# Optimization experiments

Measured on AMD Instinct MI355X. Metric: run time of the kernel, lower is better.

The kernel has to match this reference:

```python
import jax, jax.numpy as jnp
import numpy as np

D_MODEL = 1024
N_HEADS = 16
D_K = D_MODEL // N_HEADS


def setup_inputs() -> dict:
    key = jax.random.key(0)
    ks = jax.random.split(key, 7)
    B, S, D = 2, 2048, D_MODEL
    scale = 1.0 / np.sqrt(D)
    return {
        "query": jax.random.normal(ks[0], (B, S, D), dtype=jnp.float32),
        "key": jax.random.normal(ks[1], (B, S, D), dtype=jnp.float32),
        "value": jax.random.normal(ks[2], (B, S, D), dtype=jnp.float32),
        "w_q": jax.random.normal(ks[3], (D, D), dtype=jnp.float32) * scale,
        "w_k": jax.random.normal(ks[4], (D, D), dtype=jnp.float32) * scale,
        "w_v": jax.random.normal(ks[5], (D, D), dtype=jnp.float32) * scale,
        "w_o": jax.random.normal(ks[6], (D, D), dtype=jnp.float32) * scale,
    }


def reference(query, key, value, w_q, w_k, w_v, w_o):
    B, S, D = query.shape
    H, Dk = N_HEADS, D_K
    # nn.Linear (no bias): x @ W.T ; then split heads -> [B, H, S, Dk]
    def split_heads(x, W):
        return (x @ W.T).reshape(B, S, H, Dk).transpose(0, 2, 1, 3)
    Q = split_heads(query, w_q)
    K = split_heads(key, w_k)
    V = split_heads(value, w_v)
    scores = jnp.einsum("bhqd,bhkd->bhqk", Q, K) / np.sqrt(Dk).astype(jnp.float32)
    attn = jax.nn.softmax(scores, axis=-1)  # dropout is identity in eval
    attended = jnp.einsum("bhqk,bhkd->bhqd", attn, V)
    attended = attended.transpose(0, 2, 1, 3).reshape(B, S, D)
    output = attended @ w_o.T
    avg_attention = attn.mean(axis=1)  # mean over heads -> [B, S, S]
    return (output, avg_attention)
```

## Files before the change

### kernel.cpp

```cpp
#include <hip/hip_runtime.h>
#include <math.h>

#define SEQ 2048
#define DMODEL 1024
#define NH 16
#define DK 64
#define BATCH 2

using bf16x8 = __attribute__((ext_vector_type(8))) __bf16;
using bf16x4 = __attribute__((ext_vector_type(4))) __bf16;
using f32x4  = __attribute__((ext_vector_type(4))) float;

__device__ inline f32x4 mfma16(bf16x8 a, bf16x8 b, f32x4 c) {
    return __builtin_amdgcn_mfma_f32_16x16x32_bf16(a, b, c, 0, 0, 0);
}

__device__ inline void load_lds16(const void* g, void* l) {
    __builtin_amdgcn_global_load_lds(
        (const __attribute__((address_space(1))) void*)g,
        (__attribute__((address_space(3))) void*)l, 16, 0, 0);
}

#define VMCNT(n) asm volatile("s_waitcnt vmcnt(" #n ")" ::: "memory")
#define BARRIER() __builtin_amdgcn_s_barrier()
#define CFENCE() asm volatile("" ::: "memory")
#define EXP_SCALE 0.18033688011112042f
#define EXP2(x) __builtin_amdgcn_exp2f(x)

__global__ __launch_bounds__(256) void conv_bf16(
        const float* __restrict__ q, const float* __restrict__ k,
        const float* __restrict__ v, const float* __restrict__ wq,
        const float* __restrict__ wk, const float* __restrict__ wv,
        const float* __restrict__ wo,
        __bf16* __restrict__ oq, __bf16* __restrict__ ok, __bf16* __restrict__ ov,
        __bf16* __restrict__ owq, __bf16* __restrict__ owk,
        __bf16* __restrict__ owv, __bf16* __restrict__ owo) {
    int bid = blockIdx.x;
    const float* src;
    __bf16* dst;
    size_t off;
    if (bid < 3072) {
        int ti = bid >> 10;
        src = ti == 0 ? q : (ti == 1 ? k : v);
        dst = ti == 0 ? oq : (ti == 1 ? ok : ov);
        off = (size_t)(bid & 1023) * 4096;
    } else {
        int ti = (bid - 3072) >> 8;
        src = ti == 0 ? wq : (ti == 1 ? wk : (ti == 2 ? wv : wo));
        dst = ti == 0 ? owq : (ti == 1 ? owk : (ti == 2 ? owv : owo));
        off = (size_t)((bid - 3072) & 255) * 4096;
    }
    src += off; dst += off;
    const int t = threadIdx.x;
#pragma unroll
    for (int i = 0; i < 4; ++i) {
        float4 x = *(const float4*)(src + t * 4 + i * 1024);
        bf16x4 y;
        y[0] = (__bf16)x.x; y[1] = (__bf16)x.y;
        y[2] = (__bf16)x.z; y[3] = (__bf16)x.w;
        *(bf16x4*)(dst + t * 4 + i * 1024) = y;
    }
}

__device__ __forceinline__ void gemm_core(const __bf16* __restrict__ A,
                                          const __bf16* __restrict__ B,
                                          void* __restrict__ out, int mode,
                                          int m0, int n0, int N,
                                          __bf16* As, __bf16* Bs) {
    const int t    = threadIdx.x;
    const int w    = t >> 6;
    const int lane = t & 63;
    const int m    = lane & 15;
    const int kg   = lane >> 4;
    const int wr   = w >> 1, wc = w & 1;

    auto stage = [&](int buf, int k0) {
        const __bf16* ga0 = A + (size_t)(m0 + w * 16 + m) * 1024 + k0 + kg * 8;
        load_lds16(ga0, &As[buf * 4096 + w * 512]);
        const __bf16* ga1 = A + (size_t)(m0 + (w + 4) * 16 + m) * 1024 + k0 + kg * 8;
        load_lds16(ga1, &As[buf * 4096 + (w + 4) * 512]);
        const __bf16* gb0 = B + (size_t)(n0 + w * 16 + m) * 1024 + k0 + kg * 8;
        load_lds16(gb0, &Bs[buf * 4096 + w * 512]);
        const __bf16* gb1 = B + (size_t)(n0 + (w + 4) * 16 + m) * 1024 + k0 + kg * 8;
        load_lds16(gb1, &Bs[buf * 4096 + (w + 4) * 512]);
    };

    f32x4 acc[4][4] = {};

    stage(0, 0);
    CFENCE();
    stage(1, 32);

    int cb = 0, sb = 2;
    for (int ts = 0; ts < 32; ++ts) {
        if (ts < 30) {
            stage(sb, (ts + 2) * 32);
            VMCNT(8);
        } else if (ts == 30) {
            VMCNT(4);
        } else {
            VMCNT(0);
        }
        BARRIER();
        CFENCE();
        const __bf16* Ac = &As[cb * 4096];
        const __bf16* Bc = &Bs[cb * 4096];
        bf16x8 af[4], bg[4];
#pragma unroll
        for (int i = 0; i < 4; ++i)
            af[i] = *(const bf16x8*)&Ac[(wr * 4 + i) * 512 + lane * 8];
#pragma unroll
        for (int j = 0; j < 4; ++j)
            bg[j] = *(const bf16x8*)&Bc[(wc * 4 + j) * 512 + lane * 8];
        __builtin_amdgcn_s_setprio(1);
#pragma unroll
        for (int i = 0; i < 4; ++i)
#pragma unroll
            for (int j = 0; j < 4; ++j)
                acc[i][j] = mfma16(af[i], bg[j], acc[i][j]);
        __builtin_amdgcn_s_setprio(0);
        BARRIER();
        cb = cb == 2 ? 0 : cb + 1;
        sb = sb == 2 ? 0 : sb + 1;
    }

#pragma unroll
    for (int i = 0; i < 4; ++i) {
        const int rb = m0 + wr * 64 + i * 16 + kg * 4;
#pragma unroll
        for (int j = 0; j < 4; ++j) {
            const int gc = n0 + wc * 64 + j * 16 + m;
#pragma unroll
            for (int r = 0; r < 4; ++r) {
                const int gr = rb + r;
                const float vv = acc[i][j][r];
                if (mode == 0) {
                    ((float*)out)[(size_t)gr * N + gc] = vv;
                } else if (mode == 1) {
                    ((__bf16*)out)[(size_t)gr * N + gc] = (__bf16)vv;
                } else {
                    const int hh = gr >> 6, dd = gr & 63;
                    const int bb = gc >> 11, ss = gc & 2047;
                    ((__bf16*)out)[(((size_t)bb * NH + hh) * DK + dd) * SEQ + ss] = (__bf16)vv;
                }
            }
        }
    }
}

__device__ __forceinline__ int xcd_swz(int s, int cpx) {
    return (s & 7) * cpx + (s >> 3);
}

__global__ __launch_bounds__(256, 3) void gemm_qkv(
        const __bf16* __restrict__ Xq, const __bf16* __restrict__ Wq, __bf16* Qr,
        const __bf16* __restrict__ Xk, const __bf16* __restrict__ Wk, __bf16* Kr,
        const __bf16* __restrict__ Xv, const __bf16* __restrict__ Wv, __bf16* Vt) {
    __shared__ __align__(16) __bf16 As[12288];
    __shared__ __align__(16) __bf16 Bs[12288];
    const int bid = blockIdx.x;
    if (bid < 256) {
        const int s = xcd_swz(bid, 32);
        gemm_core(Xq, Wq, Qr, 1, (s >> 3) * 128, (s & 7) * 128, 1024, As, Bs);
    } else if (bid < 512) {
        const int s = xcd_swz(bid - 256, 32);
        gemm_core(Xk, Wk, Kr, 1, (s >> 3) * 128, (s & 7) * 128, 1024, As, Bs);
    } else {
        const int s = xcd_swz(bid - 512, 32);
        gemm_core(Wv, Xv, Vt, 2, (s >> 5) * 128, (s & 31) * 128, 4096, As, Bs);
    }
}

__global__ __launch_bounds__(256, 4) void attn_flash(const __bf16* __restrict__ Qr,
                                                     const __bf16* __restrict__ Kr,
                                                     const __bf16* __restrict__ Vt,
                                                     __bf16* __restrict__ att,
                                                     float* __restrict__ invs) {
    __shared__ __align__(16) unsigned char smem[32768];
    __bf16* Kb = (__bf16*)smem;
    __bf16* Vb = Kb + 8192;

    const int t    = threadIdx.x;
    const int w    = t >> 6;
    const int lane = t & 63;
    const int m    = lane & 15;
    const int kg   = lane >> 4;

    const int L  = xcd_swz(blockIdx.x, 128);
    const int b  = L >> 9;
    const int h  = (L >> 5) & 15;
    const int qw = (L & 31) * 64 + w * 16;

    const __bf16* Kh = Kr + (size_t)b * SEQ * 1024 + h * 64;
    const __bf16* Vh = Vt + ((size_t)b * NH + h) * DK * SEQ;

    const size_t rowQ = (size_t)(b * SEQ + qw + m) * 1024 + h * 64 + kg * 8;
    const bf16x8 qa = *(const bf16x8*)(Qr + rowQ);
    const bf16x8 qb = *(const bf16x8*)(Qr + rowQ + 32);
    CFENCE();

    auto kaddr = [&](int bk, int kt) {
        const int p = bk >> 1, dh = bk & 1, i = lane & 15;
        const int key = (p >> 1) * 32 + ((i >> 2) * 8) + (p & 1) * 4 + (i & 3);
        return (const void*)(Kh + (size_t)(kt + key) * 1024 + dh * 32 + (lane >> 4) * 8);
    };
    auto vaddr = [&](int bk, int kt) {
        const int nt = bk >> 1, kv = bk & 1, i = lane & 15;
        return (const void*)(Vh + (size_t)(nt * 16 + i) * SEQ + kt + kv * 32 + (lane >> 4) * 8);
    };
    auto stage = [&](int buf, int kt) {
        load_lds16(kaddr(w, kt),     Kb + buf * 4096 + w * 512);
        load_lds16(kaddr(w + 4, kt), Kb + buf * 4096 + (w + 4) * 512);
        load_lds16(vaddr(w, kt),     Vb + buf * 4096 + w * 512);
        load_lds16(vaddr(w + 4, kt), Vb + buf * 4096 + (w + 4) * 512);
    };

    f32x4 pv[4] = {};
    float rsum = 0.f;

    stage(0, 0);
    CFENCE();
    stage(1, 64);

    int cur = 0;
    for (int ts = 0; ts < 32; ++ts) {
        if (ts < 31) { VMCNT(4); } else { VMCNT(0); }
        BARRIER();
        CFENCE();
        const __bf16* Kc = Kb + cur * 4096;
        const __bf16* Vc = Vb + cur * 4096;
        bf16x4 pk[4];
#pragma unroll
        for (int p = 0; p < 4; ++p) {
            bf16x8 k0 = *(const bf16x8*)&Kc[(p * 2 + 0) * 512 + lane * 8];
            bf16x8 k1 = *(const bf16x8*)&Kc[(p * 2 + 1) * 512 + lane * 8];
            f32x4 c = {};
            c = mfma16(k0, qa, c);
            c = mfma16(k1, qb, c);
            bf16x4 t4;
#pragma unroll
            for (int r = 0; r < 4; ++r) {
                float pe = EXP2(c[r] * EXP_SCALE);
                rsum += pe;
                t4[r] = (__bf16)pe;
            }
            pk[p] = t4;
        }
#pragma unroll
        for (int ks = 0; ks < 2; ++ks) {
            bf16x8 pa;
#pragma unroll
            for (int e = 0; e < 4; ++e) {
                pa[e]     = pk[2 * ks][e];
                pa[4 + e] = pk[2 * ks + 1][e];
            }
#pragma unroll
            for (int nt = 0; nt < 4; ++nt) {
                bf16x8 vb = *(const bf16x8*)&Vc[(nt * 2 + ks) * 512 + lane * 8];
                pv[nt] = mfma16(pa, vb, pv[nt]);
            }
        }
        BARRIER();
        if (ts + 2 < 32) stage(cur, (ts + 2) * 64);
        cur ^= 1;
    }

    rsum += __shfl_xor(rsum, 16);
    rsum += __shfl_xor(rsum, 32);
    const float inv = 1.0f / rsum;
    float* sinv = (float*)(smem + 17408);
    if (lane < 16) {
        sinv[w * 16 + m] = inv;
        invs[((size_t)b * NH + h) * SEQ + qw + m] = inv;
    }
    __syncthreads();
    float iv[4];
#pragma unroll
    for (int r = 0; r < 4; ++r) iv[r] = sinv[w * 16 + kg * 4 + r];

    float* scf = (float*)smem + w * 1088;
#pragma unroll
    for (int nt = 0; nt < 4; ++nt)
#pragma unroll
        for (int r = 0; r < 4; ++r)
            scf[(kg * 4 + r) * 68 + nt * 16 + m] = pv[nt][r] * iv[r];
    __syncthreads();
    {
        const int q = lane >> 2, c0 = (lane & 3) * 16;
        const float* srcf = &scf[q * 68 + c0];
        bf16x8 o0, o1;
#pragma unroll
        for (int j = 0; j < 8; ++j) {
            o0[j] = (__bf16)srcf[j];
            o1[j] = (__bf16)srcf[j + 8];
        }
        __bf16* dst = att + (size_t)(b * SEQ + qw + q) * DMODEL + h * DK + c0;
        *(bf16x8*)(dst)     = o0;
        *(bf16x8*)(dst + 8) = o1;
    }
}

__device__ __forceinline__ void avg_core(const __bf16* __restrict__ Qr,
                                         const __bf16* __restrict__ Kr,
                                         const float* __restrict__ invs,
                                         float* __restrict__ avg,
                                         int L, __bf16* Kb) {
    const int t    = threadIdx.x;
    const int w    = t >> 6;
    const int lane = t & 63;
    const int m    = lane & 15;
    const int kg   = lane >> 4;
    const int b    = L >> 9;
    const int s0   = ((L >> 5) & 15) * 128;
    const int qw   = (L & 31) * 64 + w * 16;

    const __bf16* Kbase = Kr + (size_t)(b * SEQ + s0) * 1024;

    auto stageK = [&](int buf, int h) {
#pragma unroll
        for (int s = 0; s < 4; ++s) {
            const int bk = w * 4 + s;
            const int nt = bk >> 1, dh = bk & 1;
            load_lds16(Kbase + (size_t)(nt * 16 + (lane & 15)) * 1024 + h * 64 +
                           dh * 32 + (lane >> 4) * 8,
                       Kb + buf * 8192 + bk * 512);
        }
    };

    f32x4 acc[8] = {};

    stageK(0, 0);
    const size_t qoff = (size_t)(b * SEQ + qw + m) * 1024 + kg * 8;
    bf16x8 a0 = *(const bf16x8*)(Qr + qoff);
    bf16x8 a1 = *(const bf16x8*)(Qr + qoff + 32);
    f32x4 ivr = *(const f32x4*)&invs[(size_t)b * NH * SEQ + qw + kg * 4];
    __syncthreads();

    int cur = 0;
    for (int h = 0; h < NH; ++h) {
        if (h + 1 < NH) stageK(cur ^ 1, h + 1);
        bf16x8 na0, na1;
        f32x4 nivr;
        if (h + 1 < NH) {
            na0  = *(const bf16x8*)(Qr + qoff + (h + 1) * 64);
            na1  = *(const bf16x8*)(Qr + qoff + (h + 1) * 64 + 32);
            nivr = *(const f32x4*)&invs[((size_t)b * NH + h + 1) * SEQ + qw + kg * 4];
        }
        const __bf16* Kc = Kb + cur * 8192;
#pragma unroll
        for (int nt = 0; nt < 8; ++nt) {
            bf16x8 k0 = *(const bf16x8*)&Kc[(nt * 2 + 0) * 512 + lane * 8];
            bf16x8 k1 = *(const bf16x8*)&Kc[(nt * 2 + 1) * 512 + lane * 8];
            f32x4 c = {};
            c = mfma16(a0, k0, c);
            c = mfma16(a1, k1, c);
#pragma unroll
            for (int r = 0; r < 4; ++r)
                acc[nt][r] += ivr[r] * EXP2(c[r] * EXP_SCALE);
        }
        __syncthreads();
        cur ^= 1;
        a0 = na0; a1 = na1; ivr = nivr;
    }

    const float sc = 1.0f / NH;
#pragma unroll
    for (int nt = 0; nt < 8; ++nt)
#pragma unroll
        for (int r = 0; r < 4; ++r)
            avg[(size_t)(b * SEQ + qw + kg * 4 + r) * SEQ + s0 + nt * 16 + m] =
                acc[nt][r] * sc;
}

__global__ __launch_bounds__(256, 3) void gemm_wo_avg(
        const __bf16* __restrict__ At, const __bf16* __restrict__ Wo,
        float* __restrict__ out,
        const __bf16* __restrict__ Qr, const __bf16* __restrict__ Kr,
        const float* __restrict__ invs, float* __restrict__ avg) {
    __shared__ __align__(16) __bf16 sm[24576];
    const int bid = blockIdx.x;
    if (bid < 256) {
        const int s = xcd_swz(bid, 32);
        gemm_core(At, Wo, out, 0, (s >> 3) * 128, (s & 7) * 128, 1024,
                  sm, sm + 12288);
    } else {
        avg_core(Qr, Kr, invs, avg, xcd_swz(bid - 256, 128), sm);
    }
}

extern "C" void kernel_launch(void* const* d_in, const int* in_sizes, int n_in,
                              void* d_out, int out_size, void* d_ws, size_t ws_size,
                              hipStream_t stream) {
    const float* query = (const float*)d_in[0];
    const float* key   = (const float*)d_in[1];
    const float* value = (const float*)d_in[2];
    const float* w_q   = (const float*)d_in[3];
    const float* w_k   = (const float*)d_in[4];
    const float* w_v   = (const float*)d_in[5];
    const float* w_o   = (const float*)d_in[6];

    float* out = (float*)d_out;
    float* avg = out + (size_t)BATCH * SEQ * DMODEL;

    __bf16* Xq = (__bf16*)d_ws;
    __bf16* Xk = Xq + 4194304;
    __bf16* Xv = Xk + 4194304;
    __bf16* Wq = Xv + 4194304;
    __bf16* Wk = Wq + 1048576;
    __bf16* Wv = Wk + 1048576;
    __bf16* Wo = Wv + 1048576;
    __bf16* Qr = Wo + 1048576;
    __bf16* Kr = Qr + 4194304;
    __bf16* Vt = Kr + 4194304;
    float*  Invs = (float*)(Vt + 4194304);
    __bf16* At = Xq;

    conv_bf16<<<4096, 256, 0, stream>>>(query, key, value, w_q, w_k, w_v, w_o,
                                        Xq, Xk, Xv, Wq, Wk, Wv, Wo);

    gemm_qkv<<<768, 256, 0, stream>>>(Xq, Wq, Qr, Xk, Wk, Kr, Xv, Wv, Vt);

    attn_flash<<<1024, 256, 0, stream>>>(Qr, Kr, Vt, At, Invs);

    gemm_wo_avg<<<1280, 256, 0, stream>>>(At, Wo, out, Qr, Kr, Invs, avg);
}
```

Measured before the change: 293.8 us.

## Enlarge flash-attention tiles to 512 threads and swizzle K staging in avg kernel

The attention kernel now runs 8 waves per block covering 128 queries. It processes 128-key tiles per iteration (16 iterations instead of 32), so each staged K/V tile is shared by twice as many queries. The prefetch of the next tile is issued before the current tile's compute, and the PV MFMA phase is raised to a higher wave priority. The avg-attention kernel stages K rows in an XOR-swizzled row-major layout to reduce LDS bank conflicts. The larger shared-memory footprint of about 66KB per block will reduce how many blocks fit on each CU.

Measured after the change: 257.5 us. 1.14x faster.

```diff
diff --git a/kernel.cpp b/kernel.cpp
--- a/kernel.cpp
+++ b/kernel.cpp
@@ -171,14 +171,15 @@
     }
 }
 
-__global__ __launch_bounds__(256, 4) void attn_flash(const __bf16* __restrict__ Qr,
+__global__ __launch_bounds__(512, 4) void attn_flash(const __bf16* __restrict__ Qr,
                                                      const __bf16* __restrict__ Kr,
                                                      const __bf16* __restrict__ Vt,
                                                      __bf16* __restrict__ att,
                                                      float* __restrict__ invs) {
-    __shared__ __align__(16) unsigned char smem[32768];
-    __bf16* Kb = (__bf16*)smem;
-    __bf16* Vb = Kb + 8192;
+    __shared__ __align__(16) unsigned char smem[66048];
+    __bf16* Kb   = (__bf16*)smem;
+    __bf16* Vb   = Kb + 16384;
+    float*  sinv = (float*)(smem + 65536);
 
     const int t    = threadIdx.x;
     const int w    = t >> 6;
@@ -186,10 +187,10 @@
     const int m    = lane & 15;
     const int kg   = lane >> 4;
 
-    const int L  = xcd_swz(blockIdx.x, 128);
-    const int b  = L >> 9;
-    const int h  = (L >> 5) & 15;
-    const int qw = (L & 31) * 64 + w * 16;
+    const int L  = xcd_swz(blockIdx.x, 64);
+    const int b  = L >> 8;
+    const int h  = (L >> 4) & 15;
+    const int qw = (L & 15) * 128 + w * 16;
 
     const __bf16* Kh = Kr + (size_t)b * SEQ * 1024 + h * 64;
     const __bf16* Vh = Vt + ((size_t)b * NH + h) * DK * SEQ;
@@ -200,40 +201,43 @@
     CFENCE();
 
     auto kaddr = [&](int bk, int kt) {
-        const int p = bk >> 1, dh = bk & 1, i = lane & 15;
-        const int key = (p >> 1) * 32 + ((i >> 2) * 8) + (p & 1) * 4 + (i & 3);
+        const int f = bk >> 1, dh = bk & 1, i = lane & 15;
+        const int key = (f >> 1) * 32 + (i >> 2) * 8 + (f & 1) * 4 + (i & 3);
         return (const void*)(Kh + (size_t)(kt + key) * 1024 + dh * 32 + (lane >> 4) * 8);
     };
-    auto vaddr = [&](int bk, int kt) {
-        const int nt = bk >> 1, kv = bk & 1, i = lane & 15;
-        return (const void*)(Vh + (size_t)(nt * 16 + i) * SEQ + kt + kv * 32 + (lane >> 4) * 8);
+    auto vaddr = [&](int bv, int kt) {
+        const int nt = bv >> 2, ks = bv & 3, i = lane & 15;
+        return (const void*)(Vh + (size_t)(nt * 16 + i) * SEQ + kt + ks * 32 + (lane >> 4) * 8);
     };
     auto stage = [&](int buf, int kt) {
-        load_lds16(kaddr(w, kt),     Kb + buf * 4096 + w * 512);
-        load_lds16(kaddr(w + 4, kt), Kb + buf * 4096 + (w + 4) * 512);
-        load_lds16(vaddr(w, kt),     Vb + buf * 4096 + w * 512);
-        load_lds16(vaddr(w + 4, kt), Vb + buf * 4096 + (w + 4) * 512);
+        load_lds16(kaddr(w, kt),     Kb + buf * 8192 + w * 512);
+        load_lds16(kaddr(w + 8, kt), Kb + buf * 8192 + (w + 8) * 512);
+        load_lds16(vaddr(w, kt),     Vb + buf * 8192 + w * 512);
+        load_lds16(vaddr(w + 8, kt), Vb + buf * 8192 + (w + 8) * 512);
     };
 
     f32x4 pv[4] = {};
     float rsum = 0.f;
 
     stage(0, 0);
-    CFENCE();
-    stage(1, 64);
 
     int cur = 0;
-    for (int ts = 0; ts < 32; ++ts) {
-        if (ts < 31) { VMCNT(4); } else { VMCNT(0); }
+    for (int ts = 0; ts < 16; ++ts) {
+        if (ts + 1 < 16) {
+            stage(cur ^ 1, (ts + 1) * 128);
+            VMCNT(4);
+        } else {
+            VMCNT(0);
+        }
         BARRIER();
         CFENCE();
-        const __bf16* Kc = Kb + cur * 4096;
-        const __bf16* Vc = Vb + cur * 4096;
-        bf16x4 pk[4];
-#pragma unroll
-        for (int p = 0; p < 4; ++p) {
-            bf16x8 k0 = *(const bf16x8*)&Kc[(p * 2 + 0) * 512 + lane * 8];
-            bf16x8 k1 = *(const bf16x8*)&Kc[(p * 2 + 1) * 512 + lane * 8];
+        const __bf16* Kc = Kb + cur * 8192;
+        const __bf16* Vc = Vb + cur * 8192;
+        bf16x4 pk[8];
+#pragma unroll
+        for (int f = 0; f < 8; ++f) {
+            bf16x8 k0 = *(const bf16x8*)&Kc[(f * 2 + 0) * 512 + lane * 8];
+            bf16x8 k1 = *(const bf16x8*)&Kc[(f * 2 + 1) * 512 + lane * 8];
             f32x4 c = {};
             c = mfma16(k0, qa, c);
             c = mfma16(k1, qb, c);
@@ -244,10 +248,11 @@
                 rsum += pe;
                 t4[r] = (__bf16)pe;
             }
-            pk[p] = t4;
-        }
-#pragma unroll
-        for (int ks = 0; ks < 2; ++ks) {
+            pk[f] = t4;
+        }
+        __builtin_amdgcn_s_setprio(1);
+#pragma unroll
+        for (int ks = 0; ks < 4; ++ks) {
             bf16x8 pa;
 #pragma unroll
             for (int e = 0; e < 4; ++e) {
@@ -256,19 +261,18 @@
             }
 #pragma unroll
             for (int nt = 0; nt < 4; ++nt) {
-                bf16x8 vb = *(const bf16x8*)&Vc[(nt * 2 + ks) * 512 + lane * 8];
+                bf16x8 vb = *(const bf16x8*)&Vc[(nt * 4 + ks) * 512 + lane * 8];
                 pv[nt] = mfma16(pa, vb, pv[nt]);
             }
         }
+        __builtin_amdgcn_s_setprio(0);
         BARRIER();
-        if (ts + 2 < 32) stage(cur, (ts + 2) * 64);
         cur ^= 1;
     }
 
     rsum += __shfl_xor(rsum, 16);
     rsum += __shfl_xor(rsum, 32);
     const float inv = 1.0f / rsum;
-    float* sinv = (float*)(smem + 17408);
     if (lane < 16) {
         sinv[w * 16 + m] = inv;
         invs[((size_t)b * NH + h) * SEQ + qw + m] = inv;
@@ -319,11 +323,11 @@
     auto stageK = [&](int buf, int h) {
 #pragma unroll
         for (int s = 0; s < 4; ++s) {
-            const int bk = w * 4 + s;
-            const int nt = bk >> 1, dh = bk & 1;
-            load_lds16(Kbase + (size_t)(nt * 16 + (lane & 15)) * 1024 + h * 64 +
-                           dh * 32 + (lane >> 4) * 8,
-                       Kb + buf * 8192 + bk * 512);
+            const int i   = w * 4 + s;
+            const int row = i * 8 + (lane >> 3);
+            const int u   = lane & 7;
+            load_lds16(Kbase + (size_t)row * 1024 + h * 64 + ((u ^ (row & 7)) * 8),
+                       Kb + buf * 8192 + i * 512);
         }
     };
 
@@ -349,8 +353,9 @@
         const __bf16* Kc = Kb + cur * 8192;
 #pragma unroll
         for (int nt = 0; nt < 8; ++nt) {
-            bf16x8 k0 = *(const bf16x8*)&Kc[(nt * 2 + 0) * 512 + lane * 8];
-            bf16x8 k1 = *(const bf16x8*)&Kc[(nt * 2 + 1) * 512 + lane * 8];
+            const int row = nt * 16 + m;
+            bf16x8 k0 = *(const bf16x8*)&Kc[row * 64 + ((kg ^ (m & 7)) * 8)];
+            bf16x8 k1 = *(const bf16x8*)&Kc[row * 64 + (((kg + 4) ^ (m & 7)) * 8)];
             f32x4 c = {};
             c = mfma16(a0, k0, c);
             c = mfma16(a1, k1, c);
@@ -420,7 +425,7 @@
 
     gemm_qkv<<<768, 256, 0, stream>>>(Xq, Wq, Qr, Xk, Wk, Kr, Xv, Wv, Vt);
 
-    attn_flash<<<1024, 256, 0, stream>>>(Qr, Kr, Vt, At, Invs);
+    attn_flash<<<512, 512, 0, stream>>>(Qr, Kr, Vt, At, Invs);
 
     gemm_wo_avg<<<1280, 256, 0, stream>>>(At, Wo, out, Qr, Kr, Invs, avg);
 }
```
